# Optimization experiments

Hardware: AMD Instinct MI355X
Metric: run time of the kernel (lower is better)

## Reference

```python
import jax, jax.numpy as jnp
import numpy as np

B, N, HD = 128, 8192, 256


def setup_inputs() -> dict:
    key = jax.random.key(0)
    ks = jax.random.split(key, 12)
    s = 1.0 / np.sqrt(HD)
    return {
        "encoder_outputs": jax.random.normal(ks[0], (B, N, HD), jnp.float32),
        "hidden": jax.random.normal(ks[1], (B, HD), jnp.float32),
        "cell": jax.random.normal(ks[2], (B, HD), jnp.float32),
        "end_node_embed": jax.random.normal(ks[3], (1, HD), jnp.float32),
        "initial_input": jax.random.normal(ks[4], (B, 3 * HD), jnp.float32),
        # LSTMCell params (PyTorch layout: gates ordered i, f, g, o)
        "W_ih": jax.random.uniform(ks[5], (4 * HD, 3 * HD), jnp.float32, -s, s),
        "b_ih": jax.random.uniform(ks[6], (4 * HD,), jnp.float32, -s, s),
        "W_hh": jax.random.uniform(ks[7], (4 * HD, HD), jnp.float32, -s, s),
        "b_hh": jax.random.uniform(ks[8], (4 * HD,), jnp.float32, -s, s),
        # query_transform Linear params
        "Wq": jax.random.uniform(ks[9], (HD, HD), jnp.float32, -s, s),
        "bq": jax.random.uniform(ks[10], (HD,), jnp.float32, -s, s),
        "max_steps": 10,
    }


def reference(encoder_outputs, hidden, cell, end_node_embed, initial_input,
              W_ih, b_ih, W_hh, b_hh, Wq, bq, max_steps):
    # Prediction mode (teacher_indices=None): feed back top-3 gathered embeddings.
    def step(carry, _):
        h, c, x = carry
        gates = x @ W_ih.T + b_ih + h @ W_hh.T + b_hh        # (B, 4*HD)
        i, f, g, o = jnp.split(gates, 4, axis=-1)
        c_new = jax.nn.sigmoid(f) * c + jax.nn.sigmoid(i) * jnp.tanh(g)
        h_new = jax.nn.sigmoid(o) * jnp.tanh(c_new)
        query = h_new @ Wq.T + bq                            # (B, HD)
        logits = jnp.einsum('bd,bnd->bn', query, encoder_outputs)  # (B, N)
        _, top3 = jax.lax.top_k(logits, 3)                   # (B, 3) int32
        vecs = jnp.take_along_axis(encoder_outputs, top3[..., None], axis=1)  # (B, 3, HD)
        x_next = vecs.reshape(x.shape[0], -1)                # (B, 3*HD)
        return (h_new, c_new, x_next), (logits, top3)
    _, (logits_all, idx_all) = jax.lax.scan(
        step, (hidden, cell, initial_input), None, length=max_steps)
    return logits_all, idx_all  # (max_steps, B, N), (max_steps, B, 3)
```

## Files before the change

kernel.cpp:

```cpp
#include <hip/hip_runtime.h>

typedef unsigned short u16;
typedef unsigned int   u32;

#define B_    128
#define N_    8192
#define HD_   256
#define X_    768
#define T_    10
#define SEGS_ 16
#define SEGROWS_ 512

__device__ float g_h[B_*HD_];
__device__ float g_c[B_*HD_];
__device__ float g_q[B_*HD_];
__device__ float g_pval[B_*SEGS_*3];
__device__ int   g_pidx[B_*SEGS_*3];
__device__ int   g_isf32;

struct P {
  const void *enc, *h0, *c0, *x0, *Wih, *bih, *Whh, *bhh, *Wq, *bq;
  void* out;
};

__device__ __forceinline__ float bf2f(u16 u){ return __uint_as_float(((u32)u)<<16); }
__device__ __forceinline__ float lo2f(u32 w){ return __uint_as_float(w<<16); }
__device__ __forceinline__ float hi2f(u32 w){ return __uint_as_float(w & 0xffff0000u); }
__device__ __forceinline__ u16 f2bf(float f){
  u32 u = __float_as_uint(f);
  u32 r = u + 0x7fffu + ((u>>16)&1u);
  return (u16)(r>>16);
}

template<bool F32>
__device__ __forceinline__ float ld1(const void* p, size_t i){
  if constexpr (F32) return ((const float*)p)[i];
  else               return bf2f(((const u16*)p)[i]);
}

template<bool F32>
__device__ __forceinline__ void st1(void* p, size_t i, float v){
  if constexpr (F32) ((float*)p)[i] = v;
  else               ((u16*)p)[i]   = f2bf(v);
}

template<bool F32>
__device__ __forceinline__ void ld8(const void* p, size_t i, float* o){
  if constexpr (F32){
    const float4* q = (const float4*)((const float*)p + i);
    float4 a = q[0], b = q[1];
    o[0]=a.x; o[1]=a.y; o[2]=a.z; o[3]=a.w;
    o[4]=b.x; o[5]=b.y; o[6]=b.z; o[7]=b.w;
  } else {
    uint4 u = *(const uint4*)((const u16*)p + i);
    o[0]=lo2f(u.x); o[1]=hi2f(u.x); o[2]=lo2f(u.y); o[3]=hi2f(u.y);
    o[4]=lo2f(u.z); o[5]=hi2f(u.z); o[6]=lo2f(u.w); o[7]=hi2f(u.w);
  }
}

template<bool F32> struct Raw8 { uint4 a; };
template<> struct Raw8<true>   { uint4 a, b; };

template<bool F32>
__device__ __forceinline__ void ldraw(const void* p, size_t i, Raw8<F32>& r){
  if constexpr (F32){
    const uint4* q = (const uint4*)((const float*)p + i);
    r.a = q[0]; r.b = q[1];
  } else {
    r.a = *(const uint4*)((const u16*)p + i);
  }
}

template<bool F32>
__device__ __forceinline__ void cvt8(const Raw8<F32>& r, float* o){
  if constexpr (F32){
    o[0]=__uint_as_float(r.a.x); o[1]=__uint_as_float(r.a.y);
    o[2]=__uint_as_float(r.a.z); o[3]=__uint_as_float(r.a.w);
    o[4]=__uint_as_float(r.b.x); o[5]=__uint_as_float(r.b.y);
    o[6]=__uint_as_float(r.b.z); o[7]=__uint_as_float(r.b.w);
  } else {
    o[0]=lo2f(r.a.x); o[1]=hi2f(r.a.x); o[2]=lo2f(r.a.y); o[3]=hi2f(r.a.y);
    o[4]=lo2f(r.a.z); o[5]=hi2f(r.a.z); o[6]=lo2f(r.a.w); o[7]=hi2f(r.a.w);
  }
}

__device__ __forceinline__ void t3ins(float v,int i,
    float&v0,int&i0,float&v1,int&i1,float&v2,int&i2){
  if (v>v0 || (v==v0 && i<i0)) { v2=v1;i2=i1; v1=v0;i1=i0; v0=v;i0=i; }
  else if (v>v1 || (v==v1 && i<i1)) { v2=v1;i2=i1; v1=v;i1=i; }
  else if (v>v2 || (v==v2 && i<i2)) { v2=v;i2=i; }
}

__global__ void k_probe(const void* enc){
  const int lane = threadIdx.x;
  const u16 u = ((const u16*)enc)[lane*2];
  const float a = fabsf(bf2f(u));
  const bool inr = (a >= 0.0009765625f) && (a <= 1024.0f);
  unsigned long long m = __ballot(inr ? 1 : 0);
  if (lane==0) g_isf32 = (__popcll(m) < 32) ? 1 : 0;
}

template<bool F32>
__device__ void lstm_b(const P& p, int t, int b)
{
  const int d = threadIdx.x;
  __shared__ float xs[X_];
  __shared__ float hs[HD_];
  __shared__ float hn[HD_];
  __shared__ int   idx3[3];

  float cd;
  if (t == 0){
    for (int i=d;i<X_;i+=256) xs[i] = ld1<F32>(p.x0, (size_t)b*X_+i);
    hs[d] = ld1<F32>(p.h0, (size_t)b*HD_+d);
    cd    = ld1<F32>(p.c0, (size_t)b*HD_+d);
  } else {
    if (d==0){
      float v0=-3.4e38f,v1=-3.4e38f,v2=-3.4e38f; int i0=-1,i1=-1,i2=-1;
      const float* pv = g_pval + b*SEGS_*3;
      const int*   pi = g_pidx + b*SEGS_*3;
      for (int s=0;s<SEGS_*3;s++) t3ins(pv[s],pi[s],v0,i0,v1,i1,v2,i2);
      idx3[0]=i0; idx3[1]=i1; idx3[2]=i2;
      const size_t ib = (size_t)T_*B_*N_ + (size_t)(t-1)*B_*3 + (size_t)b*3;
      st1<F32>(p.out, ib+0, (float)i0);
      st1<F32>(p.out, ib+1, (float)i1);
      st1<F32>(p.out, ib+2, (float)i2);
    }
    __syncthreads();
    #pragma unroll
    for (int j=0;j<3;j++){
      int jj = idx3[j]; jj = jj<0 ? 0 : (jj>N_-1 ? N_-1 : jj);
      xs[j*HD_+d] = ld1<F32>(p.enc, ((size_t)b*N_ + jj)*HD_ + d);
    }
    hs[d] = g_h[b*HD_+d];
    cd    = g_c[b*HD_+d];
  }
  __syncthreads();

  float g4[4];
  #pragma unroll
  for (int gi=0;gi<4;gi++){
    const int row = gi*HD_ + d;
    float acc = ld1<F32>(p.bih,row) + ld1<F32>(p.bhh,row);
    #pragma unroll 4
    for (int kk=0;kk<X_/8;kk++){
      float w[8]; ld8<F32>(p.Wih, (size_t)row*X_ + kk*8, w);
      #pragma unroll
      for (int j=0;j<8;j++) acc = fmaf(xs[kk*8+j], w[j], acc);
    }
    #pragma unroll 4
    for (int kk=0;kk<HD_/8;kk++){
      float w[8]; ld8<F32>(p.Whh, (size_t)row*HD_ + kk*8, w);
      #pragma unroll
      for (int j=0;j<8;j++) acc = fmaf(hs[kk*8+j], w[j], acc);
    }
    g4[gi]=acc;
  }
  const float sig_i = 1.f/(1.f+expf(-g4[0]));
  const float sig_f = 1.f/(1.f+expf(-g4[1]));
  const float tan_g = tanhf(g4[2]);
  const float sig_o = 1.f/(1.f+expf(-g4[3]));
  const float cn = sig_f*cd + sig_i*tan_g;
  const float hv = sig_o*tanhf(cn);
  g_c[b*HD_+d]=cn; g_h[b*HD_+d]=hv; hn[d]=hv;
  __syncthreads();

  float acc = ld1<F32>(p.bq,d);
  #pragma unroll 4
  for (int kk=0;kk<HD_/8;kk++){
    float w[8]; ld8<F32>(p.Wq, (size_t)d*HD_ + kk*8, w);
    #pragma unroll
    for (int j=0;j<8;j++) acc = fmaf(hn[kk*8+j], w[j], acc);
  }
  g_q[b*HD_+d]=acc;
}

__global__ __launch_bounds__(256) void k_lstm(P p, int t)
{
  if (g_isf32) lstm_b<true >(p, t, blockIdx.x);
  else         lstm_b<false>(p, t, blockIdx.x);
}

template<bool F32>
__device__ void logits_b(const P& p, int t, int b, int seg)
{
  const int tid  = threadIdx.x;
  const int wave = tid>>6;
  const int lane = tid&63;
  const int oct  = lane>>3;
  const int ol   = lane&7;

  __shared__ float lbuf[SEGROWS_];
  __shared__ float sv[4][3];
  __shared__ int   si[4][3];

  float qv[4][8];
  #pragma unroll
  for (int c=0;c<4;c++){
    const float* qp = g_q + b*HD_ + ol*8 + c*64;
    #pragma unroll
    for (int j=0;j<8;j++) qv[c][j]=qp[j];
  }

  const size_t segrow = (size_t)b*N_ + (size_t)seg*SEGROWS_;
  float v0=-3.4e38f,v1=-3.4e38f,v2=-3.4e38f; int i0=-1,i1=-1,i2=-1;

  Raw8<F32> uA[4], uB[4];

  #define ROW_OF(k) ((k)*32 + wave*8 + oct)
  #define LOADR(k, u) do{                                                  \
    int r_ = ROW_OF(k) & (SEGROWS_-1);                                     \
    _Pragma("unroll")                                                      \
    for (int c_=0;c_<4;c_++)                                               \
      ldraw<F32>(p.enc, (segrow + r_)*HD_ + ol*8 + c_*64, u[c_]);          \
  }while(0)
  #define PROC(k, u) do{                                                   \
    float acc_ = 0.f;                                                      \
    _Pragma("unroll")                                                      \
    for (int c_=0;c_<4;c_++){                                              \
      float w_[8]; cvt8<F32>(u[c_], w_);                                   \
      _Pragma("unroll")                                                    \
      for (int j_=0;j_<8;j_++) acc_ = fmaf(qv[c_][j_], w_[j_], acc_);      \
    }                                                                      \
    acc_ += __shfl_xor(acc_, 1, 64);                                       \
    acc_ += __shfl_xor(acc_, 2, 64);                                       \
    acc_ += __shfl_xor(acc_, 4, 64);                                       \
    const int r_ = ROW_OF(k);                                              \
    if (ol==0) lbuf[r_] = acc_;                                            \
    const float cs_ = (ol==0) ? acc_ : -3.4e38f;                           \
    const int   ci_ = (ol==0) ? (seg*SEGROWS_ + r_) : -1;                  \
    t3ins(cs_, ci_, v0,i0,v1,i1,v2,i2);                                    \
  }while(0)

  LOADR(0, uA);
  #pragma unroll 1
  for (int k=0;k<16;k+=2){
    LOADR(k+1, uB);
    PROC(k, uA);
    if (k+2 < 16) LOADR(k+2, uA);
    PROC(k+1, uB);
  }
  #undef ROW_OF
  #undef LOADR
  #undef PROC

  #pragma unroll
  for (int d=8; d<64; d<<=1){
    float w0=__shfl_xor(v0,d,64), w1=__shfl_xor(v1,d,64), w2=__shfl_xor(v2,d,64);
    int   j0=__shfl_xor(i0,d,64), j1=__shfl_xor(i1,d,64), j2=__shfl_xor(i2,d,64);
    t3ins(w0,j0, v0,i0,v1,i1,v2,i2);
    t3ins(w1,j1, v0,i0,v1,i1,v2,i2);
    t3ins(w2,j2, v0,i0,v1,i1,v2,i2);
  }
  if (lane==0){
    sv[wave][0]=v0; sv[wave][1]=v1; sv[wave][2]=v2;
    si[wave][0]=i0; si[wave][1]=i1; si[wave][2]=i2;
  }
  __syncthreads();

  if (tid==0){
    float w0=-3.4e38f,w1=-3.4e38f,w2=-3.4e38f; int j0=-1,j1=-1,j2=-1;
    for (int s=0;s<4;s++)
      for (int k=0;k<3;k++)
        t3ins(sv[s][k],si[s][k],w0,j0,w1,j1,w2,j2);
    float* pv = g_pval + (b*SEGS_+seg)*3;
    int*   pi = g_pidx + (b*SEGS_+seg)*3;
    pv[0]=w0; pv[1]=w1; pv[2]=w2;
    pi[0]=j0; pi[1]=j1; pi[2]=j2;
  }

  const size_t obase = (size_t)t*B_*N_ + segrow;
  if constexpr (F32){
    float2* o2 = (float2*)((float*)p.out + obase);
    o2[tid] = make_float2(lbuf[2*tid], lbuf[2*tid+1]);
  } else {
    u32* o4 = (u32*)((u16*)p.out + obase);
    o4[tid] = (u32)f2bf(lbuf[2*tid]) | ((u32)f2bf(lbuf[2*tid+1])<<16);
  }
}

__global__ __launch_bounds__(256) void k_logits(P p, int t)
{
  if (g_isf32) logits_b<true >(p, t, blockIdx.y, blockIdx.x);
  else         logits_b<false>(p, t, blockIdx.y, blockIdx.x);
}

template<bool F32>
__device__ void final_b(const P& p, int b)
{
  if (threadIdx.x==0){
    float v0=-3.4e38f,v1=-3.4e38f,v2=-3.4e38f; int i0=-1,i1=-1,i2=-1;
    const float* pv = g_pval + b*SEGS_*3;
    const int*   pi = g_pidx + b*SEGS_*3;
    for (int s=0;s<SEGS_*3;s++) t3ins(pv[s],pi[s],v0,i0,v1,i1,v2,i2);
    const size_t ib = (size_t)T_*B_*N_ + (size_t)(T_-1)*B_*3 + (size_t)b*3;
    st1<F32>(p.out, ib+0, (float)i0);
    st1<F32>(p.out, ib+1, (float)i1);
    st1<F32>(p.out, ib+2, (float)i2);
  }
}

__global__ void k_final(P p)
{
  if (g_isf32) final_b<true >(p, blockIdx.x);
  else         final_b<false>(p, blockIdx.x);
}

extern "C" void kernel_launch(void* const* d_in, const int* in_sizes, int n_in,
                              void* d_out, int out_size, void* d_ws, size_t ws_size,
                              hipStream_t stream)
{
  (void)in_sizes; (void)n_in; (void)out_size; (void)d_ws; (void)ws_size;
  P p;
  p.enc = d_in[0];
  p.h0  = d_in[1];
  p.c0  = d_in[2];
  p.x0  = d_in[4];
  p.Wih = d_in[5];
  p.bih = d_in[6];
  p.Whh = d_in[7];
  p.bhh = d_in[8];
  p.Wq  = d_in[9];
  p.bq  = d_in[10];
  p.out = d_out;

  k_probe<<<dim3(1),dim3(64),0,stream>>>(p.enc);

  for (int t=0;t<T_;t++){
    k_lstm  <<<dim3(B_),       dim3(256),0,stream>>>(p, t);
    k_logits<<<dim3(SEGS_,B_), dim3(256),0,stream>>>(p, t);
  }
  k_final<<<dim3(B_),dim3(64),0,stream>>>(p);
}
```

Before: 4.129 ms.

## Restructure logits kernel row mapping with prefetch and 1D grid

Rewrites the logits kernel: the bf16 path uses 32 lanes per row with an 8-deep register prefetch, and the f32 path maps one thread per full row, reading q from shared memory. The grid is flattened to 1D and shared buffers move to kernel scope. The intent is to cut shuffle reductions and improve load pipelining. The f32 path now makes strided, uncoalesced per-thread row reads, which risks poor memory efficiency.

```diff
diff --git a/kernel.cpp b/kernel.cpp
--- a/kernel.cpp
+++ b/kernel.cpp
@@ -23,6 +23,11 @@
   void* out;
 };
 
+typedef u32   u32x4 __attribute__((ext_vector_type(4)));
+typedef float f32x4 __attribute__((ext_vector_type(4)));
+typedef const __attribute__((address_space(1))) u32x4* gu4;
+typedef const __attribute__((address_space(1))) f32x4* gf4;
+
 __device__ __forceinline__ float bf2f(u16 u){ return __uint_as_float(((u32)u)<<16); }
 __device__ __forceinline__ float lo2f(u32 w){ return __uint_as_float(w<<16); }
 __device__ __forceinline__ float hi2f(u32 w){ return __uint_as_float(w & 0xffff0000u); }
@@ -58,32 +63,6 @@
   }
 }
 
-template<bool F32> struct Raw8 { uint4 a; };
-template<> struct Raw8<true>   { uint4 a, b; };
-
-template<bool F32>
-__device__ __forceinline__ void ldraw(const void* p, size_t i, Raw8<F32>& r){
-  if constexpr (F32){
-    const uint4* q = (const uint4*)((const float*)p + i);
-    r.a = q[0]; r.b = q[1];
-  } else {
-    r.a = *(const uint4*)((const u16*)p + i);
-  }
-}
-
-template<bool F32>
-__device__ __forceinline__ void cvt8(const Raw8<F32>& r, float* o){
-  if constexpr (F32){
-    o[0]=__uint_as_float(r.a.x); o[1]=__uint_as_float(r.a.y);
-    o[2]=__uint_as_float(r.a.z); o[3]=__uint_as_float(r.a.w);
-    o[4]=__uint_as_float(r.b.x); o[5]=__uint_as_float(r.b.y);
-    o[6]=__uint_as_float(r.b.z); o[7]=__uint_as_float(r.b.w);
-  } else {
-    o[0]=lo2f(r.a.x); o[1]=hi2f(r.a.x); o[2]=lo2f(r.a.y); o[3]=hi2f(r.a.y);
-    o[4]=lo2f(r.a.z); o[5]=hi2f(r.a.z); o[6]=lo2f(r.a.w); o[7]=hi2f(r.a.w);
-  }
-}
-
 __device__ __forceinline__ void t3ins(float v,int i,
     float&v0,int&i0,float&v1,int&i1,float&v2,int&i2){
   if (v>v0 || (v==v0 && i<i0)) { v2=v1;i2=i1; v1=v0;i1=i0; v0=v;i0=i; }
@@ -101,13 +80,10 @@
 }
 
 template<bool F32>
-__device__ void lstm_b(const P& p, int t, int b)
+__device__ void lstm_b(const P& p, int t, int b, float* xs, float* hs, float* hn)
 {
   const int d = threadIdx.x;
-  __shared__ float xs[X_];
-  __shared__ float hs[HD_];
-  __shared__ float hn[HD_];
-  __shared__ int   idx3[3];
+  __shared__ int idx3[3];
 
   float cd;
   if (t == 0){
@@ -177,82 +153,102 @@
 
 __global__ __launch_bounds__(256) void k_lstm(P p, int t)
 {
-  if (g_isf32) lstm_b<true >(p, t, blockIdx.x);
-  else         lstm_b<false>(p, t, blockIdx.x);
-}
-
-template<bool F32>
-__device__ void logits_b(const P& p, int t, int b, int seg)
+  __shared__ float xs[X_], hs[HD_], hn[HD_];
+  if (g_isf32) lstm_b<true >(p, t, blockIdx.x, xs, hs, hn);
+  else         lstm_b<false>(p, t, blockIdx.x, xs, hs, hn);
+}
+
+template<bool F32>
+__device__ void logits_b(const P& p, int t, int b, int seg,
+                         float* qs, float* lbuf, float (*sv)[3], int (*si)[3])
 {
   const int tid  = threadIdx.x;
   const int wave = tid>>6;
-  const int lane = tid&63;
-  const int oct  = lane>>3;
-  const int ol   = lane&7;
-
-  __shared__ float lbuf[SEGROWS_];
-  __shared__ float sv[4][3];
-  __shared__ int   si[4][3];
-
-  float qv[4][8];
-  #pragma unroll
-  for (int c=0;c<4;c++){
-    const float* qp = g_q + b*HD_ + ol*8 + c*64;
-    #pragma unroll
-    for (int j=0;j<8;j++) qv[c][j]=qp[j];
-  }
-
-  const size_t segrow = (size_t)b*N_ + (size_t)seg*SEGROWS_;
+  const int l    = tid&63;
+  const int kl   = l&31;
+  const int half = l>>5;
+
+  for (int i=tid;i<HD_;i+=256) qs[i] = g_q[b*HD_+i];
+  __syncthreads();
+
   float v0=-3.4e38f,v1=-3.4e38f,v2=-3.4e38f; int i0=-1,i1=-1,i2=-1;
-
-  Raw8<F32> uA[4], uB[4];
-
-  #define ROW_OF(k) ((k)*32 + wave*8 + oct)
-  #define LOADR(k, u) do{                                                  \
-    int r_ = ROW_OF(k) & (SEGROWS_-1);                                     \
-    _Pragma("unroll")                                                      \
-    for (int c_=0;c_<4;c_++)                                               \
-      ldraw<F32>(p.enc, (segrow + r_)*HD_ + ol*8 + c_*64, u[c_]);          \
-  }while(0)
-  #define PROC(k, u) do{                                                   \
-    float acc_ = 0.f;                                                      \
-    _Pragma("unroll")                                                      \
-    for (int c_=0;c_<4;c_++){                                              \
-      float w_[8]; cvt8<F32>(u[c_], w_);                                   \
-      _Pragma("unroll")                                                    \
-      for (int j_=0;j_<8;j_++) acc_ = fmaf(qv[c_][j_], w_[j_], acc_);      \
-    }                                                                      \
-    acc_ += __shfl_xor(acc_, 1, 64);                                       \
-    acc_ += __shfl_xor(acc_, 2, 64);                                       \
-    acc_ += __shfl_xor(acc_, 4, 64);                                       \
-    const int r_ = ROW_OF(k);                                              \
-    if (ol==0) lbuf[r_] = acc_;                                            \
-    const float cs_ = (ol==0) ? acc_ : -3.4e38f;                           \
-    const int   ci_ = (ol==0) ? (seg*SEGROWS_ + r_) : -1;                  \
-    t3ins(cs_, ci_, v0,i0,v1,i1,v2,i2);                                    \
-  }while(0)
-
-  LOADR(0, uA);
-  #pragma unroll 1
-  for (int k=0;k<16;k+=2){
-    LOADR(k+1, uB);
-    PROC(k, uA);
-    if (k+2 < 16) LOADR(k+2, uA);
-    PROC(k+1, uB);
-  }
-  #undef ROW_OF
-  #undef LOADR
-  #undef PROC
-
-  #pragma unroll
-  for (int d=8; d<64; d<<=1){
-    float w0=__shfl_xor(v0,d,64), w1=__shfl_xor(v1,d,64), w2=__shfl_xor(v2,d,64);
-    int   j0=__shfl_xor(i0,d,64), j1=__shfl_xor(i1,d,64), j2=__shfl_xor(i2,d,64);
+  const int rowg0 = seg*SEGROWS_;
+
+  if constexpr (!F32){
+    float qv[8];
+    #pragma unroll
+    for (int j=0;j<8;j++) qv[j] = qs[kl*8+j];
+
+    const u16* encb = (const u16*)p.enc + ((size_t)b*N_ + (size_t)seg*SEGROWS_)*HD_;
+    const int wr0 = wave*128;
+    gu4 gbase = (gu4)(encb + ((size_t)(wr0 + half))*HD_ + kl*8);
+
+    u32x4 pf[8];
+    #pragma unroll
+    for (int ii=0;ii<8;ii++) pf[ii] = gbase[(size_t)ii*64];
+
+    #pragma unroll 1
+    for (int ito=0; ito<8; ++ito){
+      #pragma unroll
+      for (int ii=0;ii<8;ii++){
+        const int it = ito*8 + ii;
+        u32x4 u = pf[ii];
+        if (ito < 7) pf[ii] = gbase[(size_t)(it+8)*64];
+        float acc =       qv[0]*lo2f(u.x);
+        acc = fmaf(qv[1], hi2f(u.x), acc);
+        acc = fmaf(qv[2], lo2f(u.y), acc);
+        acc = fmaf(qv[3], hi2f(u.y), acc);
+        acc = fmaf(qv[4], lo2f(u.z), acc);
+        acc = fmaf(qv[5], hi2f(u.z), acc);
+        acc = fmaf(qv[6], lo2f(u.w), acc);
+        acc = fmaf(qv[7], hi2f(u.w), acc);
+        acc += __shfl_xor(acc, 1, 64);
+        acc += __shfl_xor(acc, 2, 64);
+        acc += __shfl_xor(acc, 4, 64);
+        acc += __shfl_xor(acc, 8, 64);
+        acc += __shfl_xor(acc, 16, 64);
+        const int row = wr0 + 2*it + half;
+        if (kl==0) lbuf[row] = acc;
+        t3ins(acc, rowg0 + row, v0,i0,v1,i1,v2,i2);
+      }
+    }
+  } else {
+    const float* encb = (const float*)p.enc + ((size_t)b*N_ + (size_t)seg*SEGROWS_)*HD_;
+    for (int row=tid; row<SEGROWS_; row+=256){
+      gf4 rp = (gf4)(encb + (size_t)row*HD_);
+      float acc = 0.f;
+      #pragma unroll 8
+      for (int k=0;k<64;k++){
+        f32x4 v = rp[k];
+        const float* qk = &qs[k*4];
+        acc = fmaf(v.x, qk[0], acc);
+        acc = fmaf(v.y, qk[1], acc);
+        acc = fmaf(v.z, qk[2], acc);
+        acc = fmaf(v.w, qk[3], acc);
+      }
+      lbuf[row] = acc;
+      t3ins(acc, rowg0 + row, v0,i0,v1,i1,v2,i2);
+    }
+  }
+
+  if constexpr (!F32){
+    if (kl!=0){ v0=v1=v2=-3.4e38f; i0=i1=i2=-1; }
+    float w0=__shfl_xor(v0,32,64), w1=__shfl_xor(v1,32,64), w2=__shfl_xor(v2,32,64);
+    int   j0=__shfl_xor(i0,32,64), j1=__shfl_xor(i1,32,64), j2=__shfl_xor(i2,32,64);
     t3ins(w0,j0, v0,i0,v1,i1,v2,i2);
     t3ins(w1,j1, v0,i0,v1,i1,v2,i2);
     t3ins(w2,j2, v0,i0,v1,i1,v2,i2);
-  }
-  if (lane==0){
+  } else {
+    #pragma unroll
+    for (int d=1; d<64; d<<=1){
+      float w0=__shfl_xor(v0,d,64), w1=__shfl_xor(v1,d,64), w2=__shfl_xor(v2,d,64);
+      int   j0=__shfl_xor(i0,d,64), j1=__shfl_xor(i1,d,64), j2=__shfl_xor(i2,d,64);
+      t3ins(w0,j0, v0,i0,v1,i1,v2,i2);
+      t3ins(w1,j1, v0,i0,v1,i1,v2,i2);
+      t3ins(w2,j2, v0,i0,v1,i1,v2,i2);
+    }
+  }
+  if (l==0){
     sv[wave][0]=v0; sv[wave][1]=v1; sv[wave][2]=v2;
     si[wave][0]=i0; si[wave][1]=i1; si[wave][2]=i2;
   }
@@ -269,20 +265,26 @@
     pi[0]=j0; pi[1]=j1; pi[2]=j2;
   }
 
-  const size_t obase = (size_t)t*B_*N_ + segrow;
-  if constexpr (F32){
+  const size_t obase = (size_t)t*B_*N_ + (size_t)b*N_ + (size_t)seg*SEGROWS_;
+  if constexpr (!F32){
+    u32* o4 = (u32*)((u16*)p.out + obase);
+    o4[tid] = (u32)f2bf(lbuf[2*tid]) | ((u32)f2bf(lbuf[2*tid+1])<<16);
+  } else {
     float2* o2 = (float2*)((float*)p.out + obase);
     o2[tid] = make_float2(lbuf[2*tid], lbuf[2*tid+1]);
-  } else {
-    u32* o4 = (u32*)((u16*)p.out + obase);
-    o4[tid] = (u32)f2bf(lbuf[2*tid]) | ((u32)f2bf(lbuf[2*tid+1])<<16);
   }
 }
 
 __global__ __launch_bounds__(256) void k_logits(P p, int t)
 {
-  if (g_isf32) logits_b<true >(p, t, blockIdx.y, blockIdx.x);
-  else         logits_b<false>(p, t, blockIdx.y, blockIdx.x);
+  __shared__ float qs[HD_];
+  __shared__ float lbuf[SEGROWS_];
+  __shared__ float sv[4][3];
+  __shared__ int   si[4][3];
+  const int b   = blockIdx.x >> 4;
+  const int seg = blockIdx.x & 15;
+  if (g_isf32) logits_b<true >(p, t, b, seg, qs, lbuf, sv, si);
+  else         logits_b<false>(p, t, b, seg, qs, lbuf, sv, si);
 }
 
 template<bool F32>
@@ -327,8 +329,8 @@
   k_probe<<<dim3(1),dim3(64),0,stream>>>(p.enc);
 
   for (int t=0;t<T_;t++){
-    k_lstm  <<<dim3(B_),       dim3(256),0,stream>>>(p, t);
-    k_logits<<<dim3(SEGS_,B_), dim3(256),0,stream>>>(p, t);
+    k_lstm  <<<dim3(B_),        dim3(256),0,stream>>>(p, t);
+    k_logits<<<dim3(B_*SEGS_),  dim3(256),0,stream>>>(p, t);
   }
   k_final<<<dim3(B_),dim3(64),0,stream>>>(p);
 }
```

Result: slower. 4.320 ms (+4.6%).
